# Performance work log

Measured on AMD Instinct MI355X. Metric: run time of the kernel, lower is better.

Reference implementation:

```python
import jax, jax.numpy as jnp
import numpy as np

B, N, D, DC, R = 32, 36, 2048, 4, 512  # batch, regions, feat dim, coord dim, fusion rank


def setup_inputs() -> dict:
    key = jax.random.key(0)
    ks = jax.random.split(key, 8)
    s = lambda fan_in: 1.0 / np.sqrt(fan_in)
    return {
        "mm": jax.random.normal(ks[0], (B, N, D), dtype=jnp.float32),
        "coords": jax.random.uniform(ks[1], (B, N, DC), dtype=jnp.float32),
        "U_feat": jax.random.normal(ks[2], (D, R), dtype=jnp.float32) * s(D),
        "V_feat": jax.random.normal(ks[3], (D, R), dtype=jnp.float32) * s(D),
        "P_feat": jax.random.normal(ks[4], (R, D), dtype=jnp.float32) * s(R),
        "U_coord": jax.random.normal(ks[5], (DC, R), dtype=jnp.float32) * s(DC),
        "V_coord": jax.random.normal(ks[6], (DC, R), dtype=jnp.float32) * s(DC),
        "P_coord": jax.random.normal(ks[7], (R, D), dtype=jnp.float32) * s(R),
    }


def reference(mm, coords, U_feat, V_feat, P_feat, U_coord, V_coord, P_coord):
    # Pairwise module: build all (i, j) region pairs, fuse, max-aggregate over j.
    # Original torch code detach_()'s the gathered pair tensors -> stop_gradient here.
    mm_sg = jax.lax.stop_gradient(mm)
    coords_sg = jax.lax.stop_gradient(coords)

    # Coord fusion (MLB-style low-rank multiplicative fusion)
    uc = jnp.einsum("bnc,cr->bnr", coords_sg, U_coord)   # [B,N,R]
    vc = jnp.einsum("bnc,cr->bnr", coords_sg, V_coord)   # [B,N,R]
    zc = jax.nn.relu(uc[:, :, None, :] * vc[:, None, :, :])  # [B,N,N,R]
    Rij = jnp.einsum("bijr,rd->bijd", zc, P_coord)       # [B,N,N,D]

    # Feature fusion
    uf = jnp.einsum("bnd,dr->bnr", mm_sg, U_feat)
    vf = jnp.einsum("bnd,dr->bnr", mm_sg, V_feat)
    zf = jax.nn.relu(uf[:, :, None, :] * vf[:, None, :, :])  # [B,N,N,R]
    Rij = Rij + jnp.einsum("bijr,rd->bijd", zf, P_feat)  # [B,N,N,D]

    # agg['type'] == 'max': reduce over the second region axis (j)
    mm_new = jnp.max(Rij, axis=2)                        # [B,N,D]

    # residual
    return mm_new + mm
```

## Files before the change

### kernel.cpp

```cpp
#include <hip/hip_runtime.h>

#define BI    1152
#define NREG  36
#define DD    2048
#define RR    512
#define KK    1024
#define ZROWS (BI*NREG)
#define MBLK  288
#define NBLK  128
#define ABUF  (MBLK*32)
#define BBUF  (NBLK*32)
#define BUFE  (ABUF+BBUF)

typedef __bf16 bf16;
typedef __bf16 bf16x8 __attribute__((ext_vector_type(8)));
typedef __bf16 bf16x4 __attribute__((ext_vector_type(4)));
typedef float  f32x4  __attribute__((ext_vector_type(4)));

__device__ __forceinline__ void gl_lds16(const void* g, void* l) {
  __builtin_amdgcn_global_load_lds(
      (const __attribute__((address_space(1))) unsigned int*)g,
      (__attribute__((address_space(3))) unsigned int*)l, 16, 0, 0);
}

__global__ void k_cvt_mm(const float4* __restrict__ in, bf16x4* __restrict__ out) {
  int i = blockIdx.x * 256 + threadIdx.x;
  float4 v = in[i];
  bf16x4 o = {(bf16)v.x, (bf16)v.y, (bf16)v.z, (bf16)v.w};
  out[i] = o;
}

__global__ void k_transpose_uv(const float* __restrict__ U, const float* __restrict__ V,
                               bf16* __restrict__ UT, bf16* __restrict__ VT) {
  __shared__ float tile[32][33];
  const float* in = blockIdx.z ? V : U;
  bf16* out = blockIdx.z ? VT : UT;
  int tx = threadIdx.x, ty = threadIdx.y;
  int c0 = blockIdx.x * 32, r0 = blockIdx.y * 32;
#pragma unroll
  for (int k = 0; k < 4; k++)
    tile[ty + 8 * k][tx] = in[(long)(r0 + ty + 8 * k) * 512 + c0 + tx];
  __syncthreads();
#pragma unroll
  for (int k = 0; k < 4; k++)
    out[(long)(c0 + ty + 8 * k) * 2048 + r0 + tx] = (bf16)tile[tx][ty + 8 * k];
}

__global__ void k_transpose_pt(const float* __restrict__ Pc, const float* __restrict__ Pf,
                               bf16* __restrict__ out) {
  __shared__ float tile[32][33];
  const float* in = blockIdx.z ? Pf : Pc;
  int koff = blockIdx.z * 512;
  int tx = threadIdx.x, ty = threadIdx.y;
  int c0 = blockIdx.x * 32, r0 = blockIdx.y * 32;
#pragma unroll
  for (int k = 0; k < 4; k++)
    tile[ty + 8 * k][tx] = in[(long)(r0 + ty + 8 * k) * 2048 + c0 + tx];
  __syncthreads();
  int kc = (koff + r0) >> 5;
#pragma unroll
  for (int k = 0; k < 4; k++) {
    int d = c0 + ty + 8 * k;
    out[((long)kc * 2048 + d) * 32 + tx] = (bf16)tile[tx][ty + 8 * k];
  }
}

__global__ void k_uvcoord(const float* __restrict__ coords, const float* __restrict__ Uc,
                          const float* __restrict__ Vc, float* __restrict__ uc,
                          float* __restrict__ vc) {
  int g = blockIdx.x, t = threadIdx.x;
  float c0 = coords[g * 4 + 0], c1 = coords[g * 4 + 1];
  float c2 = coords[g * 4 + 2], c3 = coords[g * 4 + 3];
#pragma unroll
  for (int i = 0; i < 2; i++) {
    int r = t + i * 256;
    uc[g * RR + r] = c0 * Uc[r] + c1 * Uc[RR + r] + c2 * Uc[2 * RR + r] + c3 * Uc[3 * RR + r];
    vc[g * RR + r] = c0 * Vc[r] + c1 * Vc[RR + r] + c2 * Vc[2 * RR + r] + c3 * Vc[3 * RR + r];
  }
}

__launch_bounds__(256)
__global__ void k_gemm_uv(const bf16* __restrict__ mmb, const bf16* __restrict__ UT,
                          const bf16* __restrict__ VT, float* __restrict__ uf,
                          float* __restrict__ vf) {
  __shared__ bf16 As[2][2048];
  __shared__ bf16 Bs[2][2048];
  const bf16* Bmat = blockIdx.z ? VT : UT;
  float* out = blockIdx.z ? vf : uf;
  int n0 = blockIdx.x * 64, m0 = blockIdx.y * 64;
  int tid = threadIdx.x, wave = tid >> 6, lane = tid & 63;

  const bf16* gA = mmb + (long)(m0 + lane) * 2048 + wave * 8;
  const bf16* gB = Bmat + (long)(n0 + lane) * 2048 + wave * 8;

  f32x4 acc[4] = {};
  gl_lds16(gA, As[0] + wave * 512);
  gl_lds16(gB, Bs[0] + wave * 512);
  for (int k0 = 0; k0 < 2048; k0 += 32) {
    int cur = (k0 >> 5) & 1;
    __syncthreads();
    if (k0 + 32 < 2048) {
      gl_lds16(gA + k0 + 32, As[cur ^ 1] + wave * 512);
      gl_lds16(gB + k0 + 32, Bs[cur ^ 1] + wave * 512);
    }
    bf16x8 bfr = *(const bf16x8*)(Bs[cur] + (lane >> 4) * 512 + (wave * 16 + (lane & 15)) * 8);
#pragma unroll
    for (int mt = 0; mt < 4; mt++) {
      bf16x8 afr = *(const bf16x8*)(As[cur] + (lane >> 4) * 512 + (mt * 16 + (lane & 15)) * 8);
      acc[mt] = __builtin_amdgcn_mfma_f32_16x16x32_bf16(afr, bfr, acc[mt], 0, 0, 0);
    }
  }
  int col = n0 + wave * 16 + (lane & 15);
#pragma unroll
  for (int mt = 0; mt < 4; mt++)
#pragma unroll
    for (int r = 0; r < 4; r++) {
      int row = m0 + mt * 16 + (lane >> 4) * 4 + r;
      out[(long)row * RR + col] = acc[mt][r];
    }
}

__global__ void k_build_z(const float* __restrict__ uc, const float* __restrict__ vc,
                          const float* __restrict__ uf, const float* __restrict__ vf,
                          bf16* __restrict__ z) {
  __shared__ float uL[36 * 128];
  __shared__ float vL[36 * 128];
  int kq = blockIdx.x, b = blockIdx.y, tid = threadIdx.x;
  const float* usrc = (kq < 4) ? uc : uf;
  const float* vsrc = (kq < 4) ? vc : vf;
  int kb = (kq & 3) * 128;
  for (int i = tid; i < 1152; i += 256) {
    int row = i >> 5, kk = (i & 31) * 4;
    long src = (long)(b * 36 + row) * RR + kb + kk;
    *(float4*)&uL[row * 128 + kk] = *(const float4*)(usrc + src);
    *(float4*)&vL[row * 128 + kk] = *(const float4*)(vsrc + src);
  }
  __syncthreads();
  for (int c = tid; c < 41472; c += 256) {
    int kcl = c / 10368;
    int rem = c - kcl * 10368;
    int row = rem >> 3;
    int x4 = rem & 7;
    int gl = row / 36;
    int j = row - gl * 36;
    int kl = kcl * 32 + x4 * 4;
    float4 u4 = *(const float4*)&uL[gl * 128 + kl];
    float4 v4 = *(const float4*)&vL[j * 128 + kl];
    float x0 = fmaxf(u4.x * v4.x, 0.f), x1 = fmaxf(u4.y * v4.y, 0.f);
    float x2 = fmaxf(u4.z * v4.z, 0.f), x3 = fmaxf(u4.w * v4.w, 0.f);
    bf16x4 o = {(bf16)x0, (bf16)x1, (bf16)x2, (bf16)x3};
    *(bf16x4*)(z + ((long)(kq * 4 + kcl) * ZROWS + (long)b * 1296 + row) * 32 + x4 * 4) = o;
  }
}

__launch_bounds__(256, 2)
__global__ void k_main(const bf16* __restrict__ z, const bf16* __restrict__ PTt,
                       const float* __restrict__ mm, float* __restrict__ out) {
  __shared__ bf16 lds[2 * BUFE];
  int bid = blockIdx.x;
  int x = bid & 7, dt = (bid >> 3) & 15, chunk = bid >> 7;
  int go = chunk * 8 + x;
  int d0 = dt * NBLK;
  int tid = threadIdx.x, wave = tid >> 6, lane = tid & 63;
  int l15 = lane & 15, qv = lane >> 4;
  int qp_c = qv ^ ((l15 >> 1) & 3);
  int mstrip = (wave >> 1) * 144;
  int nstrip = (wave & 1) * 64;

  const bf16* gp[7];
  int lofs[7];
  long kst[7];
  int qs = (lane & 3) ^ ((lane >> 3) & 3);
  int lroff = (lane >> 2) * 32 + qs * 8;
#pragma unroll
  for (int i = 0; i < 7; i++) {
    int s = wave + 4 * i;
    if (s < 18) {
      gp[i] = z + (long)go * (MBLK * 32) + s * 512 + lroff;
      lofs[i] = s * 512;
      kst[i] = (long)ZROWS * 32;
    } else if (s < 26) {
      int sb = s - 18;
      gp[i] = PTt + (long)d0 * 32 + sb * 512 + lroff;
      lofs[i] = ABUF + sb * 512;
      kst[i] = 2048L * 32;
    }
  }

  auto stage = [&](int buf) {
#pragma unroll
    for (int i = 0; i < 7; i++) {
      int s = wave + 4 * i;
      if (s < 26) {
        gl_lds16(gp[i], lds + buf * BUFE + lofs[i]);
        gp[i] += kst[i];
      }
    }
  };

  f32x4 acc[9][4] = {};
  stage(0);
  for (int kc = 0; kc < 32; kc++) {
    __syncthreads();
    if (kc < 31) stage((kc + 1) & 1);
    const bf16* cur = lds + (kc & 1) * BUFE;
    bf16x8 a[9], b[4];
#pragma unroll
    for (int mt = 0; mt < 9; mt++)
      a[mt] = *(const bf16x8*)(cur + (mstrip + mt * 16 + l15) * 32 + qp_c * 8);
#pragma unroll
    for (int nt = 0; nt < 4; nt++)
      b[nt] = *(const bf16x8*)(cur + ABUF + (nstrip + nt * 16 + l15) * 32 + qp_c * 8);
#pragma unroll
    for (int mt = 0; mt < 9; mt++)
#pragma unroll
      for (int nt = 0; nt < 4; nt++)
        acc[mt][nt] = __builtin_amdgcn_mfma_f32_16x16x32_bf16(a[mt], b[nt], acc[mt][nt], 0, 0, 0);
  }

#pragma unroll
  for (int nt = 0; nt < 4; nt++) {
#pragma unroll
    for (int h = 0; h < 4; h++) {
      float m1 = -3.0e38f;
#pragma unroll
      for (int mt = 0; mt < 9; mt++)
#pragma unroll
        for (int r = 0; r < 4; r++) {
          int row = mt * 16 + qv * 4 + r;
          if (row >= h * NREG && row < h * NREG + NREG) m1 = fmaxf(m1, acc[mt][nt][r]);
        }
      m1 = fmaxf(m1, __shfl_xor(m1, 16, 64));
      m1 = fmaxf(m1, __shfl_xor(m1, 32, 64));
      if (lane < 16) {
        int bi = go * 8 + (wave >> 1) * 4 + h;
        long o = (long)bi * DD + d0 + nstrip + nt * 16 + lane;
        out[o] = m1 + mm[o];
      }
    }
  }
}

extern "C" void kernel_launch(void* const* d_in, const int* in_sizes, int n_in,
                              void* d_out, int out_size, void* d_ws, size_t ws_size,
                              hipStream_t stream) {
  const float* mm     = (const float*)d_in[0];
  const float* coords = (const float*)d_in[1];
  const float* U_feat = (const float*)d_in[2];
  const float* V_feat = (const float*)d_in[3];
  const float* P_feat = (const float*)d_in[4];
  const float* U_coord= (const float*)d_in[5];
  const float* V_coord= (const float*)d_in[6];
  const float* P_coord= (const float*)d_in[7];
  float* out = (float*)d_out;

  char* ws = (char*)d_ws;
  bf16* z   = (bf16*)(ws + 0);
  bf16* PTt = (bf16*)(ws + 84934656);
  bf16* mmb = (bf16*)(ws + 89128960);
  bf16* UT  = (bf16*)(ws + 93847552);
  bf16* VT  = (bf16*)(ws + 95944704);
  float* uf = (float*)(ws + 98041856);
  float* vf = (float*)(ws + 100401152);
  float* uc = (float*)(ws + 102760448);
  float* vc = (float*)(ws + 105119744);

  k_cvt_mm<<<dim3(2304), dim3(256), 0, stream>>>((const float4*)mm, (bf16x4*)mmb);
  k_transpose_uv<<<dim3(16, 64, 2), dim3(32, 8), 0, stream>>>(U_feat, V_feat, UT, VT);
  k_transpose_pt<<<dim3(64, 16, 2), dim3(32, 8), 0, stream>>>(P_coord, P_feat, PTt);
  k_uvcoord<<<dim3(BI), dim3(256), 0, stream>>>(coords, U_coord, V_coord, uc, vc);
  k_gemm_uv<<<dim3(8, 18, 2), dim3(256), 0, stream>>>(mmb, UT, VT, uf, vf);
  k_build_z<<<dim3(8, 32), dim3(256), 0, stream>>>(uc, vc, uf, vf, z);
  k_main<<<dim3(2304), dim3(256), 0, stream>>>(z, PTt, mm, out);
}
```

Before: 288.0 us.

## Switch main GEMM to 32x32x16 MFMA with interleaved z layout and 6 waves

The z rows are reordered so that the 8 (b,i) groups are interleaved by j. Each 32-row MFMA tile then holds 4 rows of each group, and the max over j can be done per register slot. The main kernel moves from 16x16x32 to 32x32x16 bf16 MFMAs, with 6 waves per block (384 threads) and a K-split LDS layout. A small LDS pass combines partial maxima across the three M strips. The aim is fewer LDS reads per FLOP and a cheaper epilogue reduction. In exchange it adds an extra sync and shared-memory reduction step and changes occupancy.

```diff
diff --git a/kernel.cpp b/kernel.cpp
--- a/kernel.cpp
+++ b/kernel.cpp
@@ -8,14 +8,15 @@
 #define ZROWS (BI*NREG)
 #define MBLK  288
 #define NBLK  128
-#define ABUF  (MBLK*32)
-#define BBUF  (NBLK*32)
+#define ABUF  9216
+#define BBUF  4096
 #define BUFE  (ABUF+BBUF)
 
 typedef __bf16 bf16;
 typedef __bf16 bf16x8 __attribute__((ext_vector_type(8)));
 typedef __bf16 bf16x4 __attribute__((ext_vector_type(4)));
 typedef float  f32x4  __attribute__((ext_vector_type(4)));
+typedef float  f32x16 __attribute__((ext_vector_type(16)));
 
 __device__ __forceinline__ void gl_lds16(const void* g, void* l) {
   __builtin_amdgcn_global_load_lds(
@@ -149,11 +150,13 @@
     float x0 = fmaxf(u4.x * v4.x, 0.f), x1 = fmaxf(u4.y * v4.y, 0.f);
     float x2 = fmaxf(u4.z * v4.z, 0.f), x3 = fmaxf(u4.w * v4.w, 0.f);
     bf16x4 o = {(bf16)x0, (bf16)x1, (bf16)x2, (bf16)x3};
-    *(bf16x4*)(z + ((long)(kq * 4 + kcl) * ZROWS + (long)b * 1296 + row) * 32 + x4 * 4) = o;
-  }
-}
-
-__launch_bounds__(256, 2)
+    int bi = b * 36 + gl;
+    long rowp = (long)(bi >> 3) * 288 + j * 8 + (bi & 7);
+    *(bf16x4*)(z + ((long)(kq * 4 + kcl) * ZROWS + rowp) * 32 + x4 * 4) = o;
+  }
+}
+
+__launch_bounds__(384, 3)
 __global__ void k_main(const bf16* __restrict__ z, const bf16* __restrict__ PTt,
                        const float* __restrict__ mm, float* __restrict__ out) {
   __shared__ bf16 lds[2 * BUFE];
@@ -161,27 +164,27 @@
   int x = bid & 7, dt = (bid >> 3) & 15, chunk = bid >> 7;
   int go = chunk * 8 + x;
   int d0 = dt * NBLK;
-  int tid = threadIdx.x, wave = tid >> 6, lane = tid & 63;
-  int l15 = lane & 15, qv = lane >> 4;
-  int qp_c = qv ^ ((l15 >> 1) & 3);
-  int mstrip = (wave >> 1) * 144;
-  int nstrip = (wave & 1) * 64;
-
-  const bf16* gp[7];
-  int lofs[7];
-  long kst[7];
-  int qs = (lane & 3) ^ ((lane >> 3) & 3);
-  int lroff = (lane >> 2) * 32 + qs * 8;
-#pragma unroll
-  for (int i = 0; i < 7; i++) {
-    int s = wave + 4 * i;
+  int tid = threadIdx.x, wave = tid / 64, lane = tid & 63;
+  int l31 = lane & 31, hi = lane >> 5;
+  int ws = wave >> 1;
+  int nh = wave & 1;
+
+  const bf16* gp[5];
+  int lofs[5];
+  long kst[5];
+  int rlane = lane >> 1, h2 = lane & 1;
+#pragma unroll
+  for (int i = 0; i < 5; i++) {
+    int s = wave + 6 * i;
     if (s < 18) {
-      gp[i] = z + (long)go * (MBLK * 32) + s * 512 + lroff;
+      int sp = s / 9, rblk = s - sp * 9;
+      gp[i] = z + ((long)go * 288 + rblk * 32 + rlane) * 32 + sp * 16 + h2 * 8;
       lofs[i] = s * 512;
       kst[i] = (long)ZROWS * 32;
     } else if (s < 26) {
       int sb = s - 18;
-      gp[i] = PTt + (long)d0 * 32 + sb * 512 + lroff;
+      int sp = sb >> 2, nblk = sb & 3;
+      gp[i] = PTt + ((long)d0 + nblk * 32 + rlane) * 32 + sp * 16 + h2 * 8;
       lofs[i] = ABUF + sb * 512;
       kst[i] = 2048L * 32;
     }
@@ -189,8 +192,8 @@
 
   auto stage = [&](int buf) {
 #pragma unroll
-    for (int i = 0; i < 7; i++) {
-      int s = wave + 4 * i;
+    for (int i = 0; i < 5; i++) {
+      int s = wave + 6 * i;
       if (s < 26) {
         gl_lds16(gp[i], lds + buf * BUFE + lofs[i]);
         gp[i] += kst[i];
@@ -198,46 +201,52 @@
     }
   };
 
-  f32x4 acc[9][4] = {};
+  f32x16 acc[3][2] = {};
   stage(0);
   for (int kc = 0; kc < 32; kc++) {
     __syncthreads();
     if (kc < 31) stage((kc + 1) & 1);
     const bf16* cur = lds + (kc & 1) * BUFE;
-    bf16x8 a[9], b[4];
-#pragma unroll
-    for (int mt = 0; mt < 9; mt++)
-      a[mt] = *(const bf16x8*)(cur + (mstrip + mt * 16 + l15) * 32 + qp_c * 8);
-#pragma unroll
-    for (int nt = 0; nt < 4; nt++)
-      b[nt] = *(const bf16x8*)(cur + ABUF + (nstrip + nt * 16 + l15) * 32 + qp_c * 8);
-#pragma unroll
-    for (int mt = 0; mt < 9; mt++)
-#pragma unroll
-      for (int nt = 0; nt < 4; nt++)
-        acc[mt][nt] = __builtin_amdgcn_mfma_f32_16x16x32_bf16(a[mt], b[nt], acc[mt][nt], 0, 0, 0);
-  }
-
-#pragma unroll
-  for (int nt = 0; nt < 4; nt++) {
-#pragma unroll
-    for (int h = 0; h < 4; h++) {
-      float m1 = -3.0e38f;
-#pragma unroll
-      for (int mt = 0; mt < 9; mt++)
-#pragma unroll
-        for (int r = 0; r < 4; r++) {
-          int row = mt * 16 + qv * 4 + r;
-          if (row >= h * NREG && row < h * NREG + NREG) m1 = fmaxf(m1, acc[mt][nt][r]);
-        }
-      m1 = fmaxf(m1, __shfl_xor(m1, 16, 64));
-      m1 = fmaxf(m1, __shfl_xor(m1, 32, 64));
-      if (lane < 16) {
-        int bi = go * 8 + (wave >> 1) * 4 + h;
-        long o = (long)bi * DD + d0 + nstrip + nt * 16 + lane;
-        out[o] = m1 + mm[o];
-      }
-    }
+#pragma unroll
+    for (int sp = 0; sp < 2; sp++) {
+      bf16x8 a[3], b[2];
+#pragma unroll
+      for (int t = 0; t < 3; t++)
+        a[t] = *(const bf16x8*)(cur + sp * 4608 + (ws * 96 + t * 32 + l31) * 16 + hi * 8);
+#pragma unroll
+      for (int nt = 0; nt < 2; nt++)
+        b[nt] = *(const bf16x8*)(cur + ABUF + sp * 2048 + (nh * 64 + nt * 32 + l31) * 16 + hi * 8);
+#pragma unroll
+      for (int t = 0; t < 3; t++)
+#pragma unroll
+        for (int nt = 0; nt < 2; nt++)
+          acc[t][nt] = __builtin_amdgcn_mfma_f32_32x32x16_bf16(a[t], b[nt], acc[t][nt], 0, 0, 0);
+    }
+  }
+
+  float* pfp = (float*)lds;
+#pragma unroll
+  for (int nt = 0; nt < 2; nt++) {
+    int col = nh * 64 + nt * 32 + l31;
+#pragma unroll
+    for (int s0 = 0; s0 < 4; s0++) {
+      float mx = -3.0e38f;
+#pragma unroll
+      for (int t = 0; t < 3; t++)
+#pragma unroll
+        for (int rq = 0; rq < 4; rq++)
+          mx = fmaxf(mx, acc[t][nt][rq * 4 + s0]);
+      int g = s0 + 4 * hi;
+      pfp[(ws * 8 + g) * 128 + col] = mx;
+    }
+  }
+  __syncthreads();
+  for (int o = tid; o < 1024; o += 384) {
+    int g = o >> 7, col = o & 127;
+    float v = fmaxf(fmaxf(pfp[g * 128 + col], pfp[(8 + g) * 128 + col]),
+                    pfp[(16 + g) * 128 + col]);
+    long oa = (long)(go * 8 + g) * DD + d0 + col;
+    out[oa] = v + mm[oa];
   }
 }
 
@@ -271,5 +280,5 @@
   k_uvcoord<<<dim3(BI), dim3(256), 0, stream>>>(coords, U_coord, V_coord, uc, vc);
   k_gemm_uv<<<dim3(8, 18, 2), dim3(256), 0, stream>>>(mmb, UT, VT, uf, vf);
   k_build_z<<<dim3(8, 32), dim3(256), 0, stream>>>(uc, vc, uf, vf, z);
-  k_main<<<dim3(2304), dim3(256), 0, stream>>>(z, PTt, mm, out);
-}
+  k_main<<<dim3(2304), dim3(384), 0, stream>>>(z, PTt, mm, out);
+}
```

Measured after the change: 328.6 us. 1.14x slower.
